# Optimization experiments

Hardware: AMD Instinct MI355X
Metric: run time of the kernel (lower is better)

The kernel has to match this reference:

```python
import jax, jax.numpy as jnp
import numpy as np

B, L, D, H, K = 1, 1024, 512, 8, 24
h = D // H
EPS = 1e-5


def setup_inputs() -> dict:
    key = jax.random.key(0)
    ks = jax.random.split(key, 8)
    s = 0.02
    return {
        "x": jax.random.normal(ks[0], (B, L, D), jnp.float32),
        "Wq": jax.random.normal(ks[1], (D, D), jnp.float32) * s,
        "bq": jnp.zeros((D,), jnp.float32),
        "Wk": jax.random.normal(ks[2], (D, D), jnp.float32) * s,
        "bk": jnp.zeros((D,), jnp.float32),
        "Wv": jax.random.normal(ks[3], (D, D), jnp.float32) * s,
        "bv": jnp.zeros((D,), jnp.float32),
        "Wo": jax.random.normal(ks[4], (D, D), jnp.float32) * s,
        "bo": jnp.zeros((D,), jnp.float32),
        "Wg": jax.random.normal(ks[5], (h * h, 1), jnp.float32) * s,
        "bg": jnp.zeros((1,), jnp.float32),
        "kv_norm_scale": jnp.ones((1, H, 1, h, h), jnp.float32),
        "qk_norm_scale": jnp.full((1, H, 1), 1.0 / np.sqrt(h), jnp.float32),
        "spectral_filters": jax.random.normal(ks[6], (L, K), jnp.float32) * 0.1,
    }


def _full_conv(filters, u, n_fft, L_out):
    # filters: [L, K], u: [B, H, L, h] -> causal FFT conv: [B, H, L, K, h]
    Ff = jnp.fft.rfft(filters, n=n_fft, axis=0)            # [F, K]
    U = jnp.fft.rfft(u, n=n_fft, axis=2)                    # [B, H, F, h]
    y = jnp.fft.irfft(U[:, :, :, None, :] * Ff[None, None, :, :, None], n=n_fft, axis=2)
    return y[:, :, :L_out]


def reference(x, Wq, bq, Wk, bk, Wv, bv, Wo, bo, Wg, bg,
              kv_norm_scale, qk_norm_scale, spectral_filters):
    Bb, Ll, Dd = x.shape
    q = (x @ Wq + bq).reshape(Bb, Ll, H, h).transpose(0, 2, 1, 3)  # [B,H,L,h]
    k = (x @ Wk + bk).reshape(Bb, Ll, H, h).transpose(0, 2, 1, 3)
    v = (x @ Wv + bv).reshape(Bb, Ll, H, h).transpose(0, 2, 1, 3)

    sim = jnp.einsum("bhld,bhld->bhl", q, k) * qk_norm_scale       # [B,H,L]

    # F.normalize(dim=-1)
    k = k / jnp.maximum(jnp.linalg.norm(k, axis=-1, keepdims=True), 1e-12)
    v = v / jnp.maximum(jnp.linalg.norm(v, axis=-1, keepdims=True), 1e-12)

    n_fft = 2 * Ll
    k = _full_conv(spectral_filters, k, n_fft, Ll)  # [B,H,L,K,h]
    v = _full_conv(spectral_filters, v, n_fft, Ll)

    Z = jnp.einsum("bhlkd,bhlke->bhlde", v, k) * kv_norm_scale     # [B,H,L,h,h]

    logits = Z.reshape(Bb, H, Ll, h * h) @ Wg + bg                  # [B,H,L,1]
    gates = jax.nn.relu(logits) ** 2 + EPS
    gates = gates[..., None]                                        # [B,H,L,1,1]
    gated_Z = gates * Z

    # Online-softmax associative scan over L for (m, s); Z/g combine is pure add -> cumsum.
    def combine(a, b):
        m_x, s_x = a
        m_y, s_y = b
        m = jnp.maximum(m_x, m_y)
        return (m, s_x * jnp.exp(m_x - m) + s_y * jnp.exp(m_y - m))

    m_scan, s_scan = jax.lax.associative_scan(combine, (sim, jnp.ones_like(sim)), axis=2)
    Z_scan = jnp.cumsum(gated_Z, axis=2)
    g_scan = jnp.cumsum(gates, axis=2)

    softmax_w = jnp.exp(sim - m_scan)[..., None, None] / (s_scan[..., None, None] + EPS)
    gated_w = Z_scan / (g_scan + EPS)
    attn = gated_w * (1.0 + jax.nn.silu(softmax_w))                 # [B,H,L,h,h]

    ctxt = jnp.einsum("bhld,bhlde->bhle", q, attn)                  # [B,H,L,h]
    ctxt = ctxt.transpose(0, 2, 1, 3).reshape(Bb, Ll, Dd)
    return ctxt @ Wo + bo
```

## Files before the change

kernel.cpp:

```cpp
#include <hip/hip_runtime.h>
#include <math.h>

#define Hh 8
#define Ll 1024
#define KF 24
#define Dm 512
#define EPSf 1e-5f
#define LK (Ll*KF)

typedef __attribute__((ext_vector_type(8))) short sh8;
typedef __attribute__((ext_vector_type(4))) short sh4;
typedef __attribute__((ext_vector_type(4))) float f32x4;

#define OFF_QH     0
#define OFF_KN     524288
#define OFF_VN     1048576
#define OFF_SIM    1572864
#define OFF_LOGITS 1581056
#define OFF_GATES  1589248
#define OFF_FACTOR 1597440
#define OFF_VCB    1605632
#define OFF_KCB    7897088
#define OFF_QPK    14188544
#define OFF_MPK    14450688
#define OFF_WOPK   14467072
#define OFF_CPK    14598144
#define OFF_CZP    26771456
#define OFF_S0     28868608
#define OFF_CPART  29392896
#define OFF_FPK_F  26771456
#define OFF_UPK_F  27607040
#define OFF_APK_F  28131328
#define OFF_BPK_F  28393472

__device__ inline unsigned short f2bf(float x){
    unsigned int u = __float_as_uint(x);
    unsigned int r = (u + 0x7fffu + ((u>>16)&1u)) >> 16;
    return (unsigned short)r;
}
__device__ inline float bf2f(unsigned short u){ return __uint_as_float(((unsigned int)u)<<16); }
__device__ inline sh8 ld8_8B(const unsigned short* p){
    union { sh8 s; sh4 h[2]; } u;
    u.h[0] = *(const sh4*)(p);
    u.h[1] = *(const sh4*)(p+4);
    return u.s;
}

__global__ __launch_bounds__(256) void xpk_kernel(
    const float* __restrict__ x, unsigned short* __restrict__ Apk)
{
    int mb = blockIdx.x, tid = threadIdx.x;
    for (int ks=0; ks<16; ks++){
        #pragma unroll
        for (int p=0;p<2;p++){
            int e = tid + p*256;
            int lane = e>>3, j = e&7;
            int m = mb*16 + (lane&15);
            int k = ks*32 + ((lane>>4)&3)*8 + j;
            Apk[(mb*16+ks)*512 + e] = f2bf(x[m*Dm + k]);
        }
    }
}

__global__ __launch_bounds__(256) void wpk_kernel(
    const float* __restrict__ Wq, const float* __restrict__ Wk, const float* __restrict__ Wv,
    unsigned short* __restrict__ Bpk)
{
    int nb = blockIdx.x, tid = threadIdx.x;
    int n0 = nb*16;
    int mm = n0>>9;
    const float* W = (mm==0)?Wq:((mm==1)?Wk:Wv);
    int coff = n0 & 511;
    for (int ks=0; ks<16; ks++){
        #pragma unroll
        for (int p=0;p<2;p++){
            int e = tid + p*256;
            int lane = e>>3, j = e&7;
            int kk = ks*32 + ((lane>>4)&3)*8 + j;
            int col = coff + (lane&15);
            Bpk[(nb*16+ks)*512 + e] = f2bf(W[kk*Dm + col]);
        }
    }
}

__global__ __launch_bounds__(256) void wopk_kernel(
    const float* __restrict__ Wo, unsigned short* __restrict__ Bpk2)
{
    int nb = blockIdx.x, tid = threadIdx.x;
    int n0 = nb*16;
    for (int ks=0; ks<16; ks++){
        #pragma unroll
        for (int p=0;p<2;p++){
            int e = tid + p*256;
            int lane = e>>3, j = e&7;
            int kk = ks*32 + ((lane>>4)&3)*8 + j;
            Bpk2[(nb*16+ks)*512 + e] = f2bf(Wo[kk*Dm + n0 + (lane&15)]);
        }
    }
}

__global__ __launch_bounds__(256) void mpk_kernel(
    const float* __restrict__ kvs, const float* __restrict__ Wg,
    unsigned short* __restrict__ Mpk)
{
    int hd = blockIdx.x, tid = threadIdx.x;
    for (int it=0; it<16; it++){
        int idx = tid + it*256;
        int f = idx & 511, ksnb = idx >> 9;
        int nb = ksnb>>1, ks = ksnb&1;
        int lane = f>>3, j = f&7;
        int e = nb*16 + (lane&15);
        int d = ks*32 + ((lane>>4)&3)*8 + j;
        Mpk[hd*4096 + idx] = f2bf(kvs[(hd*64+e)*64 + d]*Wg[e*64+d]);
    }
}

__global__ __launch_bounds__(256) void qkvm_kernel(
    const unsigned short* __restrict__ Apk, const unsigned short* __restrict__ Bpk,
    const float* __restrict__ bq, const float* __restrict__ bk, const float* __restrict__ bv,
    float* __restrict__ qh, float* __restrict__ kn, float* __restrict__ vn)
{
    int mt = blockIdx.x, nt = blockIdx.y;
    int tid = threadIdx.x, wid = tid>>6, lane = tid&63;
    int mb = mt*4 + wid;
    f32x4 acc[4];
    #pragma unroll
    for (int nb=0;nb<4;nb++) acc[nb]=(f32x4){0.f,0.f,0.f,0.f};
    for (int ks=0; ks<16; ks++){
        sh8 a = *(const sh8*)(Apk + (mb*16+ks)*512 + lane*8);
        #pragma unroll
        for (int nb2=0;nb2<4;nb2++){
            sh8 b = *(const sh8*)(Bpk + ((nt*4+nb2)*16+ks)*512 + lane*8);
            acc[nb2] = __builtin_amdgcn_mfma_f32_16x16x32_bf16(a, b, acc[nb2], 0,0,0);
        }
    }
    int mm = nt>>3, hd = nt&7;
    const float* bias = (mm==0)?bq:((mm==1)?bk:bv);
    float* dst = (mm==0)?qh:((mm==1)?kn:vn);
    int quad = lane>>4, col = lane&15;
    #pragma unroll
    for (int nb2=0;nb2<4;nb2++){
        int d = nb2*16 + col;
        float bval = bias[hd*64+d];
        #pragma unroll
        for (int r=0;r<4;r++){
            int t = mb*16 + quad*4 + r;
            dst[(hd*Ll + t)*64 + d] = acc[nb2][r] + bval;
        }
    }
}

__global__ __launch_bounds__(256) void nse_kernel(
    const float* __restrict__ qh, const float* __restrict__ kn, const float* __restrict__ vn,
    const float* __restrict__ qks, float* __restrict__ simg,
    unsigned short* __restrict__ Upk, unsigned short* __restrict__ Qpk)
{
    int gw = blockIdx.x*4 + (threadIdx.x>>6);
    int lane = threadIdx.x & 63;
    int hd = gw>>10, t = gw&1023;
    int base = gw*64 + lane;
    float q = qh[base], k = kn[base], v = vn[base];
    float sim = q*k, k2 = k*k, v2 = v*v;
    #pragma unroll
    for (int off=32; off; off>>=1){
        sim += __shfl_xor(sim, off, 64);
        k2  += __shfl_xor(k2,  off, 64);
        v2  += __shfl_xor(v2,  off, 64);
    }
    float kfv = k * (1.f/fmaxf(sqrtf(k2), 1e-12f));
    float vfv = v * (1.f/fmaxf(sqrtf(v2), 1e-12f));
    int d = lane;
    int ST = t>>6, ks = (t>>5)&1, j = t&7;
    int frag = ks*2048 + (d>>4)*512 + (((t>>3)&3)*16 + (d&15))*8 + j;
    Upk[((hd*16) + ST)*4096 + frag]        = f2bf(vfv);
    Upk[(((8+hd)*16) + ST)*4096 + frag]    = f2bf(kfv);
    int mb = t>>4, ks2 = d>>5, j2 = d&7;
    int fl2 = ((d>>3)&3)*16 + (t&15);
    Qpk[((hd*64+mb)*2+ks2)*512 + fl2*8 + j2] = f2bf(q);
    if (lane==0) simg[gw] = sim * qks[hd];
}

__global__ __launch_bounds__(256) void fpk_kernel(
    const float* __restrict__ filt, unsigned short* __restrict__ Fpk)
{
    int kf = blockIdx.x, dslot = blockIdx.y, tid = threadIdx.x;
    unsigned short* dst = Fpk + (kf*17 + dslot)*4096;
    for (int p=0;p<16;p++){
        int e = tid + p*256;
        int j = e&7, lane = (e>>3)&63, ks = (e>>9)&1, mb = (e>>10)&3;
        int m = mb*16 + (lane&15);
        int k = ks*32 + (lane>>4)*8 + j;
        int fidx = (dslot-1)*64 + m - k;
        float v = (fidx>=0 && fidx<Ll) ? filt[fidx*KF+kf] : 0.0f;
        dst[e] = f2bf(v);
    }
}

__global__ __launch_bounds__(256,2) void convf_kernel(
    const unsigned short* __restrict__ Fpk, const unsigned short* __restrict__ Upk,
    const unsigned short* __restrict__ Mpk,
    unsigned short* __restrict__ vcb, unsigned short* __restrict__ kcb,
    float* __restrict__ logits)
{
    __shared__ unsigned short lds[18432];
    int TT = 7 - blockIdx.x;
    int kf0 = blockIdx.y*2, hd = blockIdx.z;
    int tid=threadIdx.x, wid=tid>>6, lane=tid&63;
    int hf=wid>>1, mb0=(wid&1)*2;
    int quad=lane>>4, lm=lane&15;
    const unsigned short* Fk0 = Fpk + (kf0*17)*4096;
    const unsigned short* Fk1 = Fpk + ((kf0+1)*17)*4096;
    const unsigned short* Uv = Upk + (hd*16)*4096;
    const unsigned short* Uk = Upk + ((8+hd)*16)*4096;

    f32x4 acc[2][2][2][4];
    #pragma unroll
    for (int tz=0;tz<2;tz++)
        #pragma unroll
        for (int kf=0;kf<2;kf++)
            #pragma unroll
            for (int i=0;i<2;i++)
                #pragma unroll
                for (int nb=0;nb<4;nb++) acc[tz][kf][i][nb]=(f32x4){0.f,0.f,0.f,0.f};

    int STend = 2*TT + 2;
    {
        sh8 v0=*(const sh8*)(Uv+tid*8), v1=*(const sh8*)(Uv+(tid+256)*8);
        sh8 k0=*(const sh8*)(Uk+tid*8), k1=*(const sh8*)(Uk+(tid+256)*8);
        *(sh8*)(&lds[tid*8])=v0; *(sh8*)(&lds[(tid+256)*8])=v1;
        *(sh8*)(&lds[4096+tid*8])=k0; *(sh8*)(&lds[4096+(tid+256)*8])=k1;
    }
    for (int ST=0; ST<STend; ST++){
        sh8 nv0,nv1,nk0,nk1;
        bool more = (ST+1 < STend);
        if (more){
            const unsigned short* Uvn = Uv + (ST+1)*4096;
            const unsigned short* Ukn = Uk + (ST+1)*4096;
            nv0=*(const sh8*)(Uvn+tid*8); nv1=*(const sh8*)(Uvn+(tid+256)*8);
            nk0=*(const sh8*)(Ukn+tid*8); nk1=*(const sh8*)(Ukn+(tid+256)*8);
        }
        int dslot = 2*TT + hf - ST + 1;
        sh8 a[2][2][2];
        #pragma unroll
        for (int i=0;i<2;i++)
            #pragma unroll
            for (int ks=0;ks<2;ks++){
                a[0][i][ks] = *(const sh8*)(Fk0 + dslot*4096 + (mb0+i)*1024 + ks*512 + lane*8);
                a[1][i][ks] = *(const sh8*)(Fk1 + dslot*4096 + (mb0+i)*1024 + ks*512 + lane*8);
            }
        __syncthreads();
        const unsigned short* Bb = &lds[(ST&1)*8192];
        #pragma unroll
        for (int ks=0;ks<2;ks++)
            #pragma unroll
            for (int nb=0;nb<4;nb++){
                sh8 bv = *(const sh8*)(Bb + ks*2048 + nb*512 + lane*8);
                sh8 bk = *(const sh8*)(Bb + 4096 + ks*2048 + nb*512 + lane*8);
                #pragma unroll
                for (int kf=0;kf<2;kf++)
                    #pragma unroll
                    for (int i=0;i<2;i++){
                        acc[0][kf][i][nb] = __builtin_amdgcn_mfma_f32_16x16x32_bf16(
                            a[kf][i][ks], bv, acc[0][kf][i][nb], 0,0,0);
                        acc[1][kf][i][nb] = __builtin_amdgcn_mfma_f32_16x16x32_bf16(
                            a[kf][i][ks], bk, acc[1][kf][i][nb], 0,0,0);
                    }
            }
        if (more){
            unsigned short* Bn = &lds[((ST+1)&1)*8192];
            *(sh8*)(Bn+tid*8)=nv0; *(sh8*)(Bn+(tid+256)*8)=nv1;
            *(sh8*)(Bn+4096+tid*8)=nk0; *(sh8*)(Bn+4096+(tid+256)*8)=nk1;
        }
    }
    float logacc[2][4];
    #pragma unroll
    for (int i2=0;i2<2;i2++)
        #pragma unroll
        for (int r=0;r<4;r++) logacc[i2][r]=0.f;
    const unsigned short* mbp = Mpk + hd*4096;
    #pragma unroll
    for (int kf=0;kf<2;kf++){
        __syncthreads();
        #pragma unroll
        for (int tz=0;tz<2;tz++)
            #pragma unroll
            for (int i=0;i<2;i++)
                #pragma unroll
                for (int nb=0;nb<4;nb++)
                    #pragma unroll
                    for (int r=0;r<4;r++){
                        int tl = hf*64 + (mb0+i)*16 + quad*4 + r;
                        lds[tz*9216 + tl*72 + nb*16 + lm] = f2bf(acc[tz][kf][i][nb][r]);
                    }
        __syncthreads();
        #pragma unroll
        for (int tz=0;tz<2;tz++){
            unsigned short* dst = tz ? kcb : vcb;
            #pragma unroll
            for (int it=0; it<4; it++){
                int idx = tid + it*256;
                int row = idx>>3, seg = idx&7;
                sh8 v = *(const sh8*)(&lds[tz*9216 + row*72 + seg*8]);
                *(sh8*)(dst + ((hd*Ll + TT*128 + row)*KF + kf0+kf)*64 + seg*8) = v;
            }
        }
        f32x4 accp[2][4];
        #pragma unroll
        for (int i2=0;i2<2;i2++)
            #pragma unroll
            for (int nb=0;nb<4;nb++) accp[i2][nb]=(f32x4){0.f,0.f,0.f,0.f};
        #pragma unroll
        for (int i2=0;i2<2;i2++)
            #pragma unroll
            for (int ks=0;ks<2;ks++){
                sh8 a2 = *(const sh8*)(&lds[9216 + (wid*32+i2*16+lm)*72 + ks*32 + quad*8]);
                #pragma unroll
                for (int nb=0;nb<4;nb++){
                    sh8 bm = *(const sh8*)(mbp + (nb*2+ks)*512 + lane*8);
                    accp[i2][nb] = __builtin_amdgcn_mfma_f32_16x16x32_bf16(a2, bm, accp[i2][nb], 0,0,0);
                }
            }
        #pragma unroll
        for (int i2=0;i2<2;i2++)
            #pragma unroll
            for (int r=0;r<4;r++){
                int row_l = wid*32 + i2*16 + quad*4 + r;
                float s = 0.f;
                #pragma unroll
                for (int nb=0;nb<4;nb++)
                    s += accp[i2][nb][r]*bf2f(lds[row_l*72 + nb*16 + lm]);
                logacc[i2][r] += s;
            }
    }
    #pragma unroll
    for (int i2=0;i2<2;i2++)
        #pragma unroll
        for (int r=0;r<4;r++){
            float s = logacc[i2][r];
            s += __shfl_xor(s, 1, 64);
            s += __shfl_xor(s, 2, 64);
            s += __shfl_xor(s, 4, 64);
            s += __shfl_xor(s, 8, 64);
            if (lm==0){
                int row_l = wid*32 + i2*16 + quad*4 + r;
                atomicAdd(&logits[hd*Ll + TT*128 + row_l], s);
            }
        }
}

__global__ __launch_bounds__(256) void scan_kernel(
    const float* __restrict__ simg, const float* __restrict__ logits,
    const float* __restrict__ bg, float* __restrict__ gates, float* __restrict__ factor)
{
    int hd=blockIdx.x, tid=threadIdx.x;
    __shared__ float sm[256], ssc[256], sg[256];
    float bgv = bg[0];
    float simv[4], m_loc[4], s_loc[4], g_loc[4];
    float m = -__builtin_inff(), s = 0.f, g = 0.f;
    for(int e=0;e<4;e++){
        int ix = hd*Ll + tid*4 + e;
        simv[e] = simg[ix];
        float lg = logits[ix] + bgv;
        float r = fmaxf(lg, 0.f);
        float gv = r*r + EPSf;
        gates[ix] = gv;
        float mn = fmaxf(m, simv[e]);
        s = s*__expf(m-mn) + __expf(simv[e]-mn);
        m = mn; g += gv;
        m_loc[e]=m; s_loc[e]=s; g_loc[e]=g;
    }
    sm[tid]=m; ssc[tid]=s; sg[tid]=g;
    __syncthreads();
    for(int off=1; off<256; off<<=1){
        float pm=0, ps=0, pg=0; bool has = (tid>=off);
        if(has){ pm=sm[tid-off]; ps=ssc[tid-off]; pg=sg[tid-off]; }
        __syncthreads();
        if(has){
            float mn=fmaxf(pm, sm[tid]);
            float sn=ps*__expf(pm-mn) + ssc[tid]*__expf(sm[tid]-mn);
            sm[tid]=mn; ssc[tid]=sn; sg[tid]=pg+sg[tid];
        }
        __syncthreads();
    }
    float pm=-__builtin_inff(), ps=0.f, pg=0.f;
    if (tid>0){ pm=sm[tid-1]; ps=ssc[tid-1]; pg=sg[tid-1]; }
    for(int e=0;e<4;e++){
        float mn=fmaxf(pm, m_loc[e]);
        float sn=ps*__expf(pm-mn) + s_loc[e]*__expf(m_loc[e]-mn);
        float gn=pg + g_loc[e];
        float sw = __expf(simv[e]-mn)/(sn+EPSf);
        float silu = sw/(1.f+__expf(-sw));
        factor[hd*Ll + tid*4 + e] = (1.f+silu)/(gn+EPSf);
    }
}

#define VTS 68
#define ASS 72
__global__ __launch_bounds__(256) void p3cz_kernel(
    const unsigned short* __restrict__ Qpk,
    const unsigned short* __restrict__ vcb, const unsigned short* __restrict__ kcb,
    const float* __restrict__ gates, float* __restrict__ cpart, float* __restrict__ czp)
{
    __shared__ unsigned short VT[64*VTS];
    __shared__ unsigned short KT[64*VTS];
    __shared__ unsigned short As[4][16*ASS];
    __shared__ float gl[16];
    int tid=threadIdx.x, w=tid>>6, lane=tid&63;
    int quad=lane>>4, lm=lane&15;
    int c=blockIdx.x, qq=blockIdx.y, hd=blockIdx.z;
    int T0=c*64, tq0=T0+qq*16, RQ0=tq0*KF;
    if (tid<16) gl[tid]=gates[hd*Ll+tq0+tid];
    sh8 aq[2];
    {
        const unsigned short* qb = Qpk + ((hd*64 + (c*4+w))*2)*512;
        aq[0] = *(const sh8*)(qb + lane*8);
        aq[1] = *(const sh8*)(qb + 512 + lane*8);
    }
    f32x4 ctx[4], cz[4];
    #pragma unroll
    for (int nb=0;nb<4;nb++){ ctx[nb]=(f32x4){0,0,0,0}; cz[nb]=(f32x4){0,0,0,0}; }
    int t_g = T0 + w*16 + quad*4;
    int rp = tid>>3, e0 = (tid&7)*8, r0 = rp*2;

    for (int sub=0; sub<6; sub++){
        int RB = RQ0 + sub*64;
        const unsigned short* vrow = vcb + (hd*LK + RB)*64;
        const unsigned short* krow = kcb + (hd*LK + RB)*64;
        __syncthreads();
        {
            float g0 = gl[(RB + r0)/KF - tq0];
            float g1 = gl[(RB + r0 + 1)/KF - tq0];
            sh8 v0 = *(const sh8*)(vrow + r0*64 + e0);
            sh8 v1 = *(const sh8*)(vrow + (r0+1)*64 + e0);
            sh8 k0 = *(const sh8*)(krow + r0*64 + e0);
            sh8 k1 = *(const sh8*)(krow + (r0+1)*64 + e0);
            #pragma unroll
            for (int j=0;j<8;j++){
                unsigned int pv = (unsigned int)f2bf(bf2f((unsigned short)v0[j])*g0)
                                | ((unsigned int)f2bf(bf2f((unsigned short)v1[j])*g1)<<16);
                *(unsigned int*)(&VT[(e0+j)*VTS + r0]) = pv;
                unsigned int pk = (unsigned int)(unsigned short)k0[j]
                                | ((unsigned int)(unsigned short)k1[j]<<16);
                *(unsigned int*)(&KT[(e0+j)*VTS + r0]) = pk;
            }
        }
        f32x4 S[4];
        #pragma unroll
        for (int nb=0;nb<4;nb++) S[nb]=(f32x4){0,0,0,0};
        #pragma unroll
        for (int ks=0;ks<2;ks++){
            #pragma unroll
            for (int nb=0;nb<4;nb++){
                sh8 b = *(const sh8*)(vrow + (nb*16+lm)*64 + ks*32 + quad*8);
                S[nb] = __builtin_amdgcn_mfma_f32_16x16x32_bf16(aq[ks], b, S[nb], 0,0,0);
            }
        }
        #pragma unroll
        for (int nb=0;nb<4;nb++){
            int row_l = nb*16+lm;
            int tp = (RB + row_l)/KF;
            float g = gl[tp - tq0];
            #pragma unroll
            for (int r=0;r<4;r++){
                float v = (t_g + r >= tp) ? S[nb][r]*g : 0.f;
                As[w][(quad*4+r)*ASS + row_l] = f2bf(v);
            }
        }
        __syncthreads();
        #pragma unroll
        for (int ks=0;ks<2;ks++){
            sh8 a2 = *(const sh8*)(&As[w][lm*ASS + ks*32 + quad*8]);
            sh8 av = ld8_8B(&VT[(w*16+lm)*VTS + ks*32 + quad*8]);
            #pragma unroll
            for (int nb=0;nb<4;nb++){
                sh8 bk = ld8_8B(&KT[(nb*16+lm)*VTS + ks*32 + quad*8]);
                ctx[nb] = __builtin_amdgcn_mfma_f32_16x16x32_bf16(a2, bk, ctx[nb], 0,0,0);
                cz[nb]  = __builtin_amdgcn_mfma_f32_16x16x32_bf16(av, bk, cz[nb], 0,0,0);
            }
        }
    }
    #pragma unroll
    for (int nb=0;nb<4;nb++){
        #pragma unroll
        for (int r=0;r<4;r++){
            cpart[((qq*8+hd)*Ll + t_g + r)*64 + nb*16+lm] = ctx[nb][r];
        }
    }
    int ob = ((hd*16+c)*4+qq)*4096;
    #pragma unroll
    for (int nb=0;nb<4;nb++){
        #pragma unroll
        for (int r=0;r<4;r++){
            czp[ob + (w*16+quad*4+r)*64 + nb*16+lm] = cz[nb][r];
        }
    }
}

__global__ __launch_bounds__(256) void s0_kernel(
    const float* __restrict__ czp, unsigned short* __restrict__ S0b)
{
    int idx = blockIdx.x*256 + threadIdx.x;
    int hd = blockIdx.y;
    int d = idx>>6, e = idx&63;
    int frag = (d>>5)*2048 + (e>>4)*512 + ((((d>>3)&3)*16) + (e&15))*8 + (d&7);
    float a = 0.f;
    for (int c=0;c<16;c++){
        S0b[(hd*16+c)*4096 + frag] = f2bf(a);
        int b = ((hd*16+c)*4)*4096 + idx;
        a += czp[b] + czp[b+4096] + czp[b+2*4096] + czp[b+3*4096];
    }
}

__global__ __launch_bounds__(256) void combine_kernel(
    const unsigned short* __restrict__ Qpk, const unsigned short* __restrict__ S0b,
    const float* __restrict__ cpart, const float* __restrict__ factor,
    unsigned short* __restrict__ Cpk)
{
    int c=blockIdx.x, hd=blockIdx.y;
    int tid=threadIdx.x, wid=tid>>6, lane=tid&63, quad=lane>>4, lm=lane&15;
    int mb = c*4 + wid;
    sh8 aq0 = *(const sh8*)(Qpk + ((hd*64+mb)*2)*512 + lane*8);
    sh8 aq1 = *(const sh8*)(Qpk + ((hd*64+mb)*2+1)*512 + lane*8);
    const unsigned short* sb = S0b + (hd*16+c)*4096;
    f32x4 acc[4];
    #pragma unroll
    for (int nb=0;nb<4;nb++) acc[nb]=(f32x4){0.f,0.f,0.f,0.f};
    #pragma unroll
    for (int ks=0;ks<2;ks++){
        sh8 a = ks ? aq1 : aq0;
        #pragma unroll
        for (int nb=0;nb<4;nb++){
            sh8 b = *(const sh8*)(sb + ks*2048 + nb*512 + lane*8);
            acc[nb] = __builtin_amdgcn_mfma_f32_16x16x32_bf16(a, b, acc[nb], 0,0,0);
        }
    }
    float fv[4];
    #pragma unroll
    for (int r=0;r<4;r++) fv[r] = factor[hd*Ll + mb*16 + quad*4 + r];
    #pragma unroll
    for (int nb=0;nb<4;nb++){
        int e = nb*16 + lm;
        int dim = hd*64 + e;
        int ks2 = dim>>5, koff = dim&31, qd = koff>>3, jj = koff&7;
        #pragma unroll
        for (int r=0;r<4;r++){
            int t = mb*16 + quad*4 + r;
            float v = acc[nb][r];
            #pragma unroll
            for (int q=0;q<4;q++) v += cpart[((q*8+hd)*Ll + t)*64 + e];
            v *= fv[r];
            Cpk[((t>>4)*16 + ks2)*512 + qd*128 + (t&15)*8 + jj] = f2bf(v);
        }
    }
}

__global__ __launch_bounds__(256) void outprojm_kernel(
    const unsigned short* __restrict__ Cpk, const unsigned short* __restrict__ Wopk,
    const float* __restrict__ bo, float* __restrict__ out)
{
    int mt=blockIdx.x, nt=blockIdx.y;
    int tid=threadIdx.x, wid=tid>>6, lane=tid&63;
    int mb=mt*4+wid;
    f32x4 acc[4];
    #pragma unroll
    for (int nb=0;nb<4;nb++) acc[nb]=(f32x4){0.f,0.f,0.f,0.f};
    for (int ks=0;ks<16;ks++){
        sh8 a = *(const sh8*)(Cpk + (mb*16+ks)*512 + lane*8);
        #pragma unroll
        for (int nb2=0;nb2<4;nb2++){
            sh8 b = *(const sh8*)(Wopk + ((nt*4+nb2)*16+ks)*512 + lane*8);
            acc[nb2] = __builtin_amdgcn_mfma_f32_16x16x32_bf16(a, b, acc[nb2], 0,0,0);
        }
    }
    int quad=lane>>4, col=lane&15;
    #pragma unroll
    for (int nb2=0;nb2<4;nb2++){
        int n = nt*64 + nb2*16 + col;
        float bval = bo[n];
        #pragma unroll
        for (int r=0;r<4;r++){
            out[(mb*16+quad*4+r)*Dm + n] = acc[nb2][r] + bval;
        }
    }
}

extern "C" void kernel_launch(void* const* d_in, const int* in_sizes, int n_in,
                              void* d_out, int out_size, void* d_ws, size_t ws_size,
                              hipStream_t stream)
{
    (void)in_sizes; (void)n_in; (void)out_size; (void)ws_size;
    const float* x   =(const float*)d_in[0];
    const float* Wq  =(const float*)d_in[1];
    const float* bq  =(const float*)d_in[2];
    const float* Wk  =(const float*)d_in[3];
    const float* bk  =(const float*)d_in[4];
    const float* Wv  =(const float*)d_in[5];
    const float* bv  =(const float*)d_in[6];
    const float* Wo  =(const float*)d_in[7];
    const float* bo  =(const float*)d_in[8];
    const float* Wg  =(const float*)d_in[9];
    const float* bg  =(const float*)d_in[10];
    const float* kvs =(const float*)d_in[11];
    const float* qks =(const float*)d_in[12];
    const float* filt=(const float*)d_in[13];
    float* ws = (float*)d_ws;
    float* qh    = ws+OFF_QH;
    float* kn    = ws+OFF_KN;
    float* vn    = ws+OFF_VN;
    float* simg  = ws+OFF_SIM;
    float* logits= ws+OFF_LOGITS;
    float* gates = ws+OFF_GATES;
    float* factor= ws+OFF_FACTOR;
    float* czp   = ws+OFF_CZP;
    float* cpart = ws+OFF_CPART;
    unsigned short* vcb  = (unsigned short*)(ws + OFF_VCB);
    unsigned short* kcb  = (unsigned short*)(ws + OFF_KCB);
    unsigned short* Qpk  = (unsigned short*)(ws + OFF_QPK);
    unsigned short* Mpk  = (unsigned short*)(ws + OFF_MPK);
    unsigned short* Wopk = (unsigned short*)(ws + OFF_WOPK);
    unsigned short* Cpk  = (unsigned short*)(ws + OFF_CPK);
    unsigned short* S0b  = (unsigned short*)(ws + OFF_S0);
    unsigned short* Fpk  = (unsigned short*)(ws + OFF_FPK_F);
    unsigned short* Upk  = (unsigned short*)(ws + OFF_UPK_F);
    unsigned short* Apk  = (unsigned short*)(ws + OFF_APK_F);
    unsigned short* Bpk  = (unsigned short*)(ws + OFF_BPK_F);
    float* out   = (float*)d_out;

    hipMemsetAsync(logits, 0, Hh*Ll*sizeof(float), stream);
    xpk_kernel    <<<dim3(64),      256,0,stream>>>(x,Apk);
    wpk_kernel    <<<dim3(96),      256,0,stream>>>(Wq,Wk,Wv,Bpk);
    qkvm_kernel   <<<dim3(16,24),   256,0,stream>>>(Apk,Bpk,bq,bk,bv,qh,kn,vn);
    nse_kernel    <<<dim3(2048),    256,0,stream>>>(qh,kn,vn,qks,simg,Upk,Qpk);
    fpk_kernel    <<<dim3(24,17),   256,0,stream>>>(filt,Fpk);
    mpk_kernel    <<<dim3(8),       256,0,stream>>>(kvs,Wg,Mpk);
    wopk_kernel   <<<dim3(32),      256,0,stream>>>(Wo,Wopk);
    convf_kernel  <<<dim3(8,12,8),  256,0,stream>>>(Fpk,Upk,Mpk,vcb,kcb,logits);
    scan_kernel   <<<dim3(8),       256,0,stream>>>(simg,logits,bg,gates,factor);
    p3cz_kernel   <<<dim3(16,4,8),  256,0,stream>>>(Qpk,vcb,kcb,gates,cpart,czp);
    s0_kernel     <<<dim3(16,8),    256,0,stream>>>(czp,S0b);
    combine_kernel<<<dim3(16,8),    256,0,stream>>>(Qpk,S0b,cpart,factor,Cpk);
    outprojm_kernel<<<dim3(16,8),   256,0,stream>>>(Cpk,Wopk,bo,out);
}
```

Before: 206.4 us.

## Merge packing kernels and rebalance causal conv into 64-row tile pairs

Five small weight/input packing kernels become one multi-role launch, which removes launch overhead. The causal convolution now builds 16-row Toeplitz filter tiles, and each block handles a pair of 64-row output tiles (15-p and p) so every block does the same amount of triangular work. The old layout gave each block a single 128-row tile with uneven work. In p3cz, V rows are staged into LDS before the MFMA reads them instead of reading global memory directly, and a barrier is moved to suit. The trade is a smaller filter tile per step and two passes of sync and epilogue per block.

```diff
diff --git a/kernel.cpp b/kernel.cpp
--- a/kernel.cpp
+++ b/kernel.cpp
@@ -46,72 +46,84 @@
     return u.s;
 }
 
-__global__ __launch_bounds__(256) void xpk_kernel(
-    const float* __restrict__ x, unsigned short* __restrict__ Apk)
-{
-    int mb = blockIdx.x, tid = threadIdx.x;
-    for (int ks=0; ks<16; ks++){
-        #pragma unroll
-        for (int p=0;p<2;p++){
-            int e = tid + p*256;
-            int lane = e>>3, j = e&7;
-            int m = mb*16 + (lane&15);
-            int k = ks*32 + ((lane>>4)&3)*8 + j;
-            Apk[(mb*16+ks)*512 + e] = f2bf(x[m*Dm + k]);
-        }
-    }
-}
-
-__global__ __launch_bounds__(256) void wpk_kernel(
+__global__ __launch_bounds__(256) void pack_all_kernel(
+    const float* __restrict__ x,
     const float* __restrict__ Wq, const float* __restrict__ Wk, const float* __restrict__ Wv,
-    unsigned short* __restrict__ Bpk)
-{
-    int nb = blockIdx.x, tid = threadIdx.x;
-    int n0 = nb*16;
-    int mm = n0>>9;
-    const float* W = (mm==0)?Wq:((mm==1)?Wk:Wv);
-    int coff = n0 & 511;
-    for (int ks=0; ks<16; ks++){
-        #pragma unroll
-        for (int p=0;p<2;p++){
-            int e = tid + p*256;
-            int lane = e>>3, j = e&7;
-            int kk = ks*32 + ((lane>>4)&3)*8 + j;
-            int col = coff + (lane&15);
-            Bpk[(nb*16+ks)*512 + e] = f2bf(W[kk*Dm + col]);
-        }
-    }
-}
-
-__global__ __launch_bounds__(256) void wopk_kernel(
-    const float* __restrict__ Wo, unsigned short* __restrict__ Bpk2)
-{
-    int nb = blockIdx.x, tid = threadIdx.x;
-    int n0 = nb*16;
-    for (int ks=0; ks<16; ks++){
-        #pragma unroll
-        for (int p=0;p<2;p++){
-            int e = tid + p*256;
-            int lane = e>>3, j = e&7;
-            int kk = ks*32 + ((lane>>4)&3)*8 + j;
-            Bpk2[(nb*16+ks)*512 + e] = f2bf(Wo[kk*Dm + n0 + (lane&15)]);
-        }
-    }
-}
-
-__global__ __launch_bounds__(256) void mpk_kernel(
-    const float* __restrict__ kvs, const float* __restrict__ Wg,
-    unsigned short* __restrict__ Mpk)
-{
-    int hd = blockIdx.x, tid = threadIdx.x;
-    for (int it=0; it<16; it++){
-        int idx = tid + it*256;
-        int f = idx & 511, ksnb = idx >> 9;
-        int nb = ksnb>>1, ks = ksnb&1;
-        int lane = f>>3, j = f&7;
-        int e = nb*16 + (lane&15);
-        int d = ks*32 + ((lane>>4)&3)*8 + j;
-        Mpk[hd*4096 + idx] = f2bf(kvs[(hd*64+e)*64 + d]*Wg[e*64+d]);
+    const float* __restrict__ Wo, const float* __restrict__ kvs, const float* __restrict__ Wg,
+    const float* __restrict__ filt,
+    unsigned short* __restrict__ Apk, unsigned short* __restrict__ Bpk,
+    unsigned short* __restrict__ Wopk, unsigned short* __restrict__ Mpk,
+    unsigned short* __restrict__ Fpk16)
+{
+    int bid = blockIdx.x, tid = threadIdx.x;
+    if (bid < 64){
+        int mb = bid;
+        for (int ks=0; ks<16; ks++){
+            #pragma unroll
+            for (int p=0;p<2;p++){
+                int e = tid + p*256;
+                int lane = e>>3, j = e&7;
+                int m = mb*16 + (lane&15);
+                int k = ks*32 + ((lane>>4)&3)*8 + j;
+                Apk[(mb*16+ks)*512 + e] = f2bf(x[m*Dm + k]);
+            }
+        }
+    } else if (bid < 160){
+        int nb = bid - 64;
+        int n0 = nb*16;
+        int mm = n0>>9;
+        const float* W = (mm==0)?Wq:((mm==1)?Wk:Wv);
+        int coff = n0 & 511;
+        for (int ks=0; ks<16; ks++){
+            #pragma unroll
+            for (int p=0;p<2;p++){
+                int e = tid + p*256;
+                int lane = e>>3, j = e&7;
+                int kk = ks*32 + ((lane>>4)&3)*8 + j;
+                Bpk[(nb*16+ks)*512 + e] = f2bf(W[kk*Dm + coff + (lane&15)]);
+            }
+        }
+    } else if (bid < 192){
+        int nb = bid - 160;
+        int n0 = nb*16;
+        for (int ks=0; ks<16; ks++){
+            #pragma unroll
+            for (int p=0;p<2;p++){
+                int e = tid + p*256;
+                int lane = e>>3, j = e&7;
+                int kk = ks*32 + ((lane>>4)&3)*8 + j;
+                Wopk[(nb*16+ks)*512 + e] = f2bf(Wo[kk*Dm + n0 + (lane&15)]);
+            }
+        }
+    } else if (bid < 200){
+        int hd = bid - 192;
+        for (int it=0; it<16; it++){
+            int idx = tid + it*256;
+            int f = idx & 511, ksnb = idx >> 9;
+            int nb = ksnb>>1, ks = ksnb&1;
+            int lane = f>>3, j = f&7;
+            int e = nb*16 + (lane&15);
+            int d = ks*32 + ((lane>>4)&3)*8 + j;
+            Mpk[hd*4096 + idx] = f2bf(kvs[(hd*64+e)*64 + d]*Wg[e*64+d]);
+        }
+    } else {
+        int b2 = bid - 200;
+        for (int ti=0; ti<16; ti++){
+            int tile = b2*16 + ti;
+            int kf = tile>>6, d16 = tile&63;
+            unsigned short* dst = Fpk16 + tile*1024;
+            #pragma unroll
+            for (int p2=0;p2<4;p2++){
+                int e = tid + p2*256;
+                int ks = e>>9, f = e&511;
+                int lane = f>>3, j = f&7;
+                int m = lane&15;
+                int k = ks*32 + ((lane>>4)&3)*8 + j;
+                int fidx = 16*d16 + m - k;
+                float v = (fidx>=0 && fidx<Ll) ? filt[fidx*KF+kf] : 0.0f;
+                dst[e] = f2bf(v);
+            }
+        }
     }
 }
 
@@ -180,74 +192,47 @@
     if (lane==0) simg[gw] = sim * qks[hd];
 }
 
-__global__ __launch_bounds__(256) void fpk_kernel(
-    const float* __restrict__ filt, unsigned short* __restrict__ Fpk)
-{
-    int kf = blockIdx.x, dslot = blockIdx.y, tid = threadIdx.x;
-    unsigned short* dst = Fpk + (kf*17 + dslot)*4096;
-    for (int p=0;p<16;p++){
-        int e = tid + p*256;
-        int j = e&7, lane = (e>>3)&63, ks = (e>>9)&1, mb = (e>>10)&3;
-        int m = mb*16 + (lane&15);
-        int k = ks*32 + (lane>>4)*8 + j;
-        int fidx = (dslot-1)*64 + m - k;
-        float v = (fidx>=0 && fidx<Ll) ? filt[fidx*KF+kf] : 0.0f;
-        dst[e] = f2bf(v);
-    }
-}
-
-__global__ __launch_bounds__(256,2) void convf_kernel(
-    const unsigned short* __restrict__ Fpk, const unsigned short* __restrict__ Upk,
-    const unsigned short* __restrict__ Mpk,
+__device__ __forceinline__ void conv_phase(
+    int T, int kf0, int hd,
+    const unsigned short* __restrict__ Fpk16,
+    const unsigned short* __restrict__ Uv, const unsigned short* __restrict__ Uk,
+    const unsigned short* __restrict__ Mh,
     unsigned short* __restrict__ vcb, unsigned short* __restrict__ kcb,
-    float* __restrict__ logits)
-{
-    __shared__ unsigned short lds[18432];
-    int TT = 7 - blockIdx.x;
-    int kf0 = blockIdx.y*2, hd = blockIdx.z;
-    int tid=threadIdx.x, wid=tid>>6, lane=tid&63;
-    int hf=wid>>1, mb0=(wid&1)*2;
-    int quad=lane>>4, lm=lane&15;
-    const unsigned short* Fk0 = Fpk + (kf0*17)*4096;
-    const unsigned short* Fk1 = Fpk + ((kf0+1)*17)*4096;
-    const unsigned short* Uv = Upk + (hd*16)*4096;
-    const unsigned short* Uk = Upk + ((8+hd)*16)*4096;
-
-    f32x4 acc[2][2][2][4];
-    #pragma unroll
-    for (int tz=0;tz<2;tz++)
-        #pragma unroll
-        for (int kf=0;kf<2;kf++)
-            #pragma unroll
-            for (int i=0;i<2;i++)
-                #pragma unroll
-                for (int nb=0;nb<4;nb++) acc[tz][kf][i][nb]=(f32x4){0.f,0.f,0.f,0.f};
-
-    int STend = 2*TT + 2;
+    float* __restrict__ logits, unsigned short* lds,
+    int tid, int w, int lane)
+{
+    int quad = lane>>4, lm = lane&15;
+    f32x4 acc[2][2][4];
+    #pragma unroll
+    for (int kf=0;kf<2;kf++)
+        #pragma unroll
+        for (int tz=0;tz<2;tz++)
+            #pragma unroll
+            for (int nb=0;nb<4;nb++) acc[kf][tz][nb]=(f32x4){0.f,0.f,0.f,0.f};
+
+    __syncthreads();
     {
         sh8 v0=*(const sh8*)(Uv+tid*8), v1=*(const sh8*)(Uv+(tid+256)*8);
         sh8 k0=*(const sh8*)(Uk+tid*8), k1=*(const sh8*)(Uk+(tid+256)*8);
         *(sh8*)(&lds[tid*8])=v0; *(sh8*)(&lds[(tid+256)*8])=v1;
         *(sh8*)(&lds[4096+tid*8])=k0; *(sh8*)(&lds[4096+(tid+256)*8])=k1;
     }
-    for (int ST=0; ST<STend; ST++){
+    for (int ST=0; ST<=T; ST++){
         sh8 nv0,nv1,nk0,nk1;
-        bool more = (ST+1 < STend);
+        bool more = (ST < T);
         if (more){
             const unsigned short* Uvn = Uv + (ST+1)*4096;
             const unsigned short* Ukn = Uk + (ST+1)*4096;
             nv0=*(const sh8*)(Uvn+tid*8); nv1=*(const sh8*)(Uvn+(tid+256)*8);
             nk0=*(const sh8*)(Ukn+tid*8); nk1=*(const sh8*)(Ukn+(tid+256)*8);
         }
-        int dslot = 2*TT + hf - ST + 1;
-        sh8 a[2][2][2];
-        #pragma unroll
-        for (int i=0;i<2;i++)
-            #pragma unroll
-            for (int ks=0;ks<2;ks++){
-                a[0][i][ks] = *(const sh8*)(Fk0 + dslot*4096 + (mb0+i)*1024 + ks*512 + lane*8);
-                a[1][i][ks] = *(const sh8*)(Fk1 + dslot*4096 + (mb0+i)*1024 + ks*512 + lane*8);
-            }
+        int d16 = 4*(T-ST) + w;
+        sh8 a[2][2];
+        #pragma unroll
+        for (int kf=0;kf<2;kf++)
+            #pragma unroll
+            for (int ks=0;ks<2;ks++)
+                a[kf][ks] = *(const sh8*)(Fpk16 + ((kf0+kf)*64 + d16)*1024 + ks*512 + lane*8);
         __syncthreads();
         const unsigned short* Bb = &lds[(ST&1)*8192];
         #pragma unroll
@@ -257,14 +242,12 @@
                 sh8 bv = *(const sh8*)(Bb + ks*2048 + nb*512 + lane*8);
                 sh8 bk = *(const sh8*)(Bb + 4096 + ks*2048 + nb*512 + lane*8);
                 #pragma unroll
-                for (int kf=0;kf<2;kf++)
-                    #pragma unroll
-                    for (int i=0;i<2;i++){
-                        acc[0][kf][i][nb] = __builtin_amdgcn_mfma_f32_16x16x32_bf16(
-                            a[kf][i][ks], bv, acc[0][kf][i][nb], 0,0,0);
-                        acc[1][kf][i][nb] = __builtin_amdgcn_mfma_f32_16x16x32_bf16(
-                            a[kf][i][ks], bk, acc[1][kf][i][nb], 0,0,0);
-                    }
+                for (int kf=0;kf<2;kf++){
+                    acc[kf][0][nb] = __builtin_amdgcn_mfma_f32_16x16x32_bf16(
+                        a[kf][ks], bv, acc[kf][0][nb], 0,0,0);
+                    acc[kf][1][nb] = __builtin_amdgcn_mfma_f32_16x16x32_bf16(
+                        a[kf][ks], bk, acc[kf][1][nb], 0,0,0);
+                }
             }
         if (more){
             unsigned short* Bn = &lds[((ST+1)&1)*8192];
@@ -272,80 +255,79 @@
             *(sh8*)(Bn+4096+tid*8)=nk0; *(sh8*)(Bn+4096+(tid+256)*8)=nk1;
         }
     }
-    float logacc[2][4];
-    #pragma unroll
-    for (int i2=0;i2<2;i2++)
-        #pragma unroll
-        for (int r=0;r<4;r++) logacc[i2][r]=0.f;
-    const unsigned short* mbp = Mpk + hd*4096;
+    float logacc[4] = {0.f,0.f,0.f,0.f};
     #pragma unroll
     for (int kf=0;kf<2;kf++){
         __syncthreads();
         #pragma unroll
         for (int tz=0;tz<2;tz++)
             #pragma unroll
-            for (int i=0;i<2;i++)
+            for (int nb=0;nb<4;nb++)
                 #pragma unroll
-                for (int nb=0;nb<4;nb++)
-                    #pragma unroll
-                    for (int r=0;r<4;r++){
-                        int tl = hf*64 + (mb0+i)*16 + quad*4 + r;
-                        lds[tz*9216 + tl*72 + nb*16 + lm] = f2bf(acc[tz][kf][i][nb][r]);
-                    }
+                for (int r=0;r<4;r++){
+                    int tl = w*16 + quad*4 + r;
+                    lds[tz*4608 + tl*72 + nb*16 + lm] = f2bf(acc[kf][tz][nb][r]);
+                }
         __syncthreads();
         #pragma unroll
         for (int tz=0;tz<2;tz++){
             unsigned short* dst = tz ? kcb : vcb;
             #pragma unroll
-            for (int it=0; it<4; it++){
+            for (int it=0; it<2; it++){
                 int idx = tid + it*256;
                 int row = idx>>3, seg = idx&7;
-                sh8 v = *(const sh8*)(&lds[tz*9216 + row*72 + seg*8]);
-                *(sh8*)(dst + ((hd*Ll + TT*128 + row)*KF + kf0+kf)*64 + seg*8) = v;
-            }
-        }
-        f32x4 accp[2][4];
-        #pragma unroll
-        for (int i2=0;i2<2;i2++)
-            #pragma unroll
-            for (int nb=0;nb<4;nb++) accp[i2][nb]=(f32x4){0.f,0.f,0.f,0.f};
-        #pragma unroll
-        for (int i2=0;i2<2;i2++)
-            #pragma unroll
-            for (int ks=0;ks<2;ks++){
-                sh8 a2 = *(const sh8*)(&lds[9216 + (wid*32+i2*16+lm)*72 + ks*32 + quad*8]);
-                #pragma unroll
-                for (int nb=0;nb<4;nb++){
-                    sh8 bm = *(const sh8*)(mbp + (nb*2+ks)*512 + lane*8);
-                    accp[i2][nb] = __builtin_amdgcn_mfma_f32_16x16x32_bf16(a2, bm, accp[i2][nb], 0,0,0);
-                }
-            }
-        #pragma unroll
-        for (int i2=0;i2<2;i2++)
-            #pragma unroll
-            for (int r=0;r<4;r++){
-                int row_l = wid*32 + i2*16 + quad*4 + r;
-                float s = 0.f;
-                #pragma unroll
-                for (int nb=0;nb<4;nb++)
-                    s += accp[i2][nb][r]*bf2f(lds[row_l*72 + nb*16 + lm]);
-                logacc[i2][r] += s;
-            }
-    }
-    #pragma unroll
-    for (int i2=0;i2<2;i2++)
+                sh8 vv = *(const sh8*)(&lds[tz*4608 + row*72 + seg*8]);
+                *(sh8*)(dst + ((hd*Ll + T*64 + row)*KF + kf0+kf)*64 + seg*8) = vv;
+            }
+        }
+        f32x4 accp[4];
+        #pragma unroll
+        for (int nb=0;nb<4;nb++) accp[nb]=(f32x4){0.f,0.f,0.f,0.f};
+        #pragma unroll
+        for (int ks=0;ks<2;ks++){
+            sh8 a2 = *(const sh8*)(&lds[4608 + (w*16+lm)*72 + ks*32 + quad*8]);
+            #pragma unroll
+            for (int nb=0;nb<4;nb++){
+                sh8 bm = *(const sh8*)(Mh + (nb*2+ks)*512 + lane*8);
+                accp[nb] = __builtin_amdgcn_mfma_f32_16x16x32_bf16(a2, bm, accp[nb], 0,0,0);
+            }
+        }
         #pragma unroll
         for (int r=0;r<4;r++){
-            float s = logacc[i2][r];
-            s += __shfl_xor(s, 1, 64);
-            s += __shfl_xor(s, 2, 64);
-            s += __shfl_xor(s, 4, 64);
-            s += __shfl_xor(s, 8, 64);
-            if (lm==0){
-                int row_l = wid*32 + i2*16 + quad*4 + r;
-                atomicAdd(&logits[hd*Ll + TT*128 + row_l], s);
-            }
-        }
+            int rloc = w*16 + quad*4 + r;
+            float s = 0.f;
+            #pragma unroll
+            for (int nb=0;nb<4;nb++)
+                s += accp[nb][r]*bf2f(lds[rloc*72 + nb*16 + lm]);
+            logacc[r] += s;
+        }
+    }
+    #pragma unroll
+    for (int r=0;r<4;r++){
+        float s = logacc[r];
+        s += __shfl_xor(s, 1, 64);
+        s += __shfl_xor(s, 2, 64);
+        s += __shfl_xor(s, 4, 64);
+        s += __shfl_xor(s, 8, 64);
+        if (lm==0)
+            atomicAdd(&logits[hd*Ll + T*64 + w*16 + quad*4 + r], s);
+    }
+}
+
+__global__ __launch_bounds__(256,2) void convf_kernel(
+    const unsigned short* __restrict__ Fpk16, const unsigned short* __restrict__ Upk,
+    const unsigned short* __restrict__ Mpk,
+    unsigned short* __restrict__ vcb, unsigned short* __restrict__ kcb,
+    float* __restrict__ logits)
+{
+    __shared__ unsigned short lds[16384];
+    int p = blockIdx.x, kf0 = blockIdx.y*2, hd = blockIdx.z;
+    int tid=threadIdx.x, w=tid>>6, lane=tid&63;
+    const unsigned short* Uv = Upk + (hd*16)*4096;
+    const unsigned short* Uk = Upk + ((8+hd)*16)*4096;
+    const unsigned short* Mh = Mpk + hd*4096;
+    conv_phase(15-p, kf0, hd, Fpk16, Uv, Uk, Mh, vcb, kcb, logits, lds, tid, w, lane);
+    conv_phase(p,    kf0, hd, Fpk16, Uv, Uk, Mh, vcb, kcb, logits, lds, tid, w, lane);
 }
 
 __global__ __launch_bounds__(256) void scan_kernel(
@@ -404,6 +386,7 @@
     __shared__ unsigned short VT[64*VTS];
     __shared__ unsigned short KT[64*VTS];
     __shared__ unsigned short As[4][16*ASS];
+    __shared__ unsigned short Vraw[64*72];
     __shared__ float gl[16];
     int tid=threadIdx.x, w=tid>>6, lane=tid&63;
     int quad=lane>>4, lm=lane&15;
@@ -434,6 +417,8 @@
             sh8 v1 = *(const sh8*)(vrow + (r0+1)*64 + e0);
             sh8 k0 = *(const sh8*)(krow + r0*64 + e0);
             sh8 k1 = *(const sh8*)(krow + (r0+1)*64 + e0);
+            *(sh8*)(&Vraw[r0*72 + e0]) = v0;
+            *(sh8*)(&Vraw[(r0+1)*72 + e0]) = v1;
             #pragma unroll
             for (int j=0;j<8;j++){
                 unsigned int pv = (unsigned int)f2bf(bf2f((unsigned short)v0[j])*g0)
@@ -444,6 +429,7 @@
                 *(unsigned int*)(&KT[(e0+j)*VTS + r0]) = pk;
             }
         }
+        __syncthreads();
         f32x4 S[4];
         #pragma unroll
         for (int nb=0;nb<4;nb++) S[nb]=(f32x4){0,0,0,0};
@@ -451,7 +437,7 @@
         for (int ks=0;ks<2;ks++){
             #pragma unroll
             for (int nb=0;nb<4;nb++){
-                sh8 b = *(const sh8*)(vrow + (nb*16+lm)*64 + ks*32 + quad*8);
+                sh8 b = *(const sh8*)(&Vraw[(nb*16+lm)*72 + ks*32 + quad*8]);
                 S[nb] = __builtin_amdgcn_mfma_f32_16x16x32_bf16(aq[ks], b, S[nb], 0,0,0);
             }
         }
@@ -466,7 +452,6 @@
                 As[w][(quad*4+r)*ASS + row_l] = f2bf(v);
             }
         }
-        __syncthreads();
         #pragma unroll
         for (int ks=0;ks<2;ks++){
             sh8 a2 = *(const sh8*)(&As[w][lm*ASS + ks*32 + quad*8]);
@@ -620,21 +605,18 @@
     unsigned short* Wopk = (unsigned short*)(ws + OFF_WOPK);
     unsigned short* Cpk  = (unsigned short*)(ws + OFF_CPK);
     unsigned short* S0b  = (unsigned short*)(ws + OFF_S0);
-    unsigned short* Fpk  = (unsigned short*)(ws + OFF_FPK_F);
+    unsigned short* Fpk16= (unsigned short*)(ws + OFF_FPK_F);
     unsigned short* Upk  = (unsigned short*)(ws + OFF_UPK_F);
     unsigned short* Apk  = (unsigned short*)(ws + OFF_APK_F);
     unsigned short* Bpk  = (unsigned short*)(ws + OFF_BPK_F);
     float* out   = (float*)d_out;
 
     hipMemsetAsync(logits, 0, Hh*Ll*sizeof(float), stream);
-    xpk_kernel    <<<dim3(64),      256,0,stream>>>(x,Apk);
-    wpk_kernel    <<<dim3(96),      256,0,stream>>>(Wq,Wk,Wv,Bpk);
+    pack_all_kernel<<<dim3(296),    256,0,stream>>>(x,Wq,Wk,Wv,Wo,kvs,Wg,filt,
+                                                    Apk,Bpk,Wopk,Mpk,Fpk16);
     qkvm_kernel   <<<dim3(16,24),   256,0,stream>>>(Apk,Bpk,bq,bk,bv,qh,kn,vn);
     nse_kernel    <<<dim3(2048),    256,0,stream>>>(qh,kn,vn,qks,simg,Upk,Qpk);
-    fpk_kernel    <<<dim3(24,17),   256,0,stream>>>(filt,Fpk);
-    mpk_kernel    <<<dim3(8),       256,0,stream>>>(kvs,Wg,Mpk);
-    wopk_kernel   <<<dim3(32),      256,0,stream>>>(Wo,Wopk);
-    convf_kernel  <<<dim3(8,12,8),  256,0,stream>>>(Fpk,Upk,Mpk,vcb,kcb,logits);
+    convf_kernel  <<<dim3(8,12,8),  256,0,stream>>>(Fpk16,Upk,Mpk,vcb,kcb,logits);
     scan_kernel   <<<dim3(8),       256,0,stream>>>(simg,logits,bg,gates,factor);
     p3cz_kernel   <<<dim3(16,4,8),  256,0,stream>>>(Qpk,vcb,kcb,gates,cpart,czp);
     s0_kernel     <<<dim3(16,8),    256,0,stream>>>(czp,S0b);
```

New measurement: 175.6 us. 14.9% less time.
